# Performance work log

Hardware: AMD Instinct MI355X
Metric: run time of the kernel (lower is better)

The kernel has to match this reference:

```python
import jax, jax.numpy as jnp
import numpy as np

N_ITEMS = 100000
N_EDGES = 800000
D = 64
N_LAYERS = 3  # config['ii_layers']


def setup_inputs() -> dict:
    key = jax.random.key(0)
    k1, k2, k3, k4 = jax.random.split(key, 4)
    rows = jax.random.randint(k1, (N_EDGES,), 0, N_ITEMS, dtype=jnp.int64 if jax.config.jax_enable_x64 else jnp.int32)
    cols = jax.random.randint(k2, (N_EDGES,), 0, N_ITEMS, dtype=jnp.int64 if jax.config.jax_enable_x64 else jnp.int32)
    vals = jax.random.uniform(k3, (N_EDGES,), dtype=jnp.float32)
    item_embeddings = jax.random.normal(k4, (N_ITEMS, D), dtype=jnp.float32)
    return {"rows": rows, "cols": cols, "vals": vals, "item_embeddings": item_embeddings}


def _spmm(rows, cols, vals, x):
    # sparse.mm(A, x) with A in COO: out[r] += vals[e] * x[c] for each edge e=(r,c)
    msgs = vals[:, None] * x[cols]            # [E, D] gathered & weighted messages
    return jax.ops.segment_sum(msgs, rows, num_segments=N_ITEMS)


def reference(rows, cols, vals, item_embeddings):
    # HyperConv: iterate SpMM, average initial + all layer outputs (fused running sum).
    acc = item_embeddings
    cur = item_embeddings
    for _ in range(N_LAYERS):
        cur = _spmm(rows, cols, vals, cur)
        acc = acc + cur
    return acc / jnp.asarray(N_LAYERS + 1, dtype=item_embeddings.dtype)
```

## Files before the change

kernel.cpp:

```cpp
#include <hip/hip_runtime.h>
#include <hip/hip_fp16.h>


#define NI 100000
#define NE 800000
#define DD 64

#define RPB  512
#define BINS ((NI + RPB - 1) / RPB)
#define EPB  2048
#define P1B  ((NE + EPB - 1) / EPB)
#define CAP  5120
#define BC   32
#define CVB  6250
#define SPLIT 4
#define RQ   (RPB / SPLIT)

typedef int   i4 __attribute__((ext_vector_type(4)));
typedef float f4 __attribute__((ext_vector_type(4)));

static __device__ __forceinline__ float2 h2f(int w) {
    __half2 h = *(__half2*)&w;
    return __half22float2(h);
}

__global__ __launch_bounds__(256) void part1_conv_k(const int* __restrict__ rows,
                                                    const int* __restrict__ cols,
                                                    const float* __restrict__ vals,
                                                    int* __restrict__ bin_cnt,
                                                    int2* __restrict__ binned,
                                                    const float4* __restrict__ x,
                                                    __half* __restrict__ xh,
                                                    int n4) {
    int t = threadIdx.x;
    if (blockIdx.x >= P1B) {
        int i = (blockIdx.x - P1B) * 256 + t;
        if (i < n4) {
            float4 v = x[i];
            __half2* dst = (__half2*)(xh + (size_t)i * 4);
            dst[0] = __floats2half2_rn(v.x, v.y);
            dst[1] = __floats2half2_rn(v.z, v.w);
        }
        return;
    }

    __shared__ int  hist[BINS];
    __shared__ int  offs[BINS];
    __shared__ int  base[BINS];
    __shared__ int  cur[BINS];
    __shared__ int  sc[256];
    __shared__ int2 stage[EPB];
    __shared__ unsigned char sbin[EPB];

    int e0   = blockIdx.x * EPB;
    int ecnt = NE - e0; if (ecnt > EPB) ecnt = EPB;

    for (int i = t; i < BINS; i += 256) { hist[i] = 0; cur[i] = 0; }
    __syncthreads();
    for (int i = t; i < ecnt; i += 256)
        atomicAdd(&hist[rows[e0 + i] >> 9], 1);
    __syncthreads();

    int hv = (t < BINS) ? hist[t] : 0;
    sc[t] = hv;
    __syncthreads();
    for (int off = 1; off < 256; off <<= 1) {
        int xv = (t >= off) ? sc[t - off] : 0;
        __syncthreads();
        sc[t] += xv;
        __syncthreads();
    }
    if (t < BINS) {
        offs[t] = sc[t] - hv;
        base[t] = hv ? atomicAdd(&bin_cnt[t], hv) : 0;
    }
    __syncthreads();

    for (int i = t; i < ecnt; i += 256) {
        int r = rows[e0 + i];
        int b = r >> 9;
        int p = offs[b] + atomicAdd(&cur[b], 1);
        stage[p] = make_int2(((r & 511) << 17) | cols[e0 + i],
                             __float_as_int(vals[e0 + i]));
        sbin[p] = (unsigned char)b;
    }
    __syncthreads();

    for (int i = t; i < ecnt; i += 256) {
        int b   = sbin[i];
        int pos = base[b] + (i - offs[b]);
        if (pos < CAP) binned[(size_t)b * CAP + pos] = stage[i];
    }
}

__global__ __launch_bounds__(256) void part2_k(const int* __restrict__ bin_cnt,
                                               const int2* __restrict__ binned,
                                               int2* __restrict__ bucket,
                                               int* __restrict__ fill) {
    __shared__ int cur[RQ];
    int t  = threadIdx.x;
    int bb = blockIdx.x >> 2;
    int q  = blockIdx.x & 3;
    for (int i = t; i < RQ; i += 256) cur[i] = 0;
    __syncthreads();
    int cnt = bin_cnt[bb];
    if (cnt > CAP) cnt = CAP;
    const int2* src = binned + (size_t)bb * CAP;
    for (int i = t; i < cnt; i += 256) {
        int2 e = src[i];
        int rl = e.x >> 17;
        if ((rl >> 7) == q) {
            int pos = atomicAdd(&cur[rl & (RQ - 1)], 1);
            if (pos < BC)
                bucket[((size_t)bb * RPB + rl) * BC + pos] =
                    make_int2(e.x & 0x1FFFF, e.y);
        }
    }
    __syncthreads();
    for (int i = t; i < RQ; i += 256) {
        int rl = q * RQ + i;
        int r  = bb * RPB + rl;
        if (r < NI) {
            int c = (cur[i] < BC) ? cur[i] : BC;
            if (c & 1) {
                bucket[((size_t)bb * RPB + rl) * BC + c] = make_int2(0, 0);
                c++;
            }
            fill[r] = c;
        }
    }
}

template <int MODE>
__global__ __launch_bounds__(256, 8) void spmm_k(const int* __restrict__ fill,
                                                 const int2* __restrict__ bucket,
                                                 const __half* __restrict__ xin,
                                                 __half* __restrict__ nxt,
                                                 const float* __restrict__ x0,
                                                 const __half* __restrict__ s1,
                                                 float* __restrict__ outp) {
    int tid  = threadIdx.x;
    int lane = tid & 63;
    int grp  = lane >> 3;
    int ll   = lane & 7;
    int r    = blockIdx.x * 32 + (tid >> 6) * 8 + grp;
    int deg  = fill[r];
    const int2* ep = bucket + (size_t)r * BC;

    int wmax = deg;
    wmax = max(wmax, __shfl_xor(wmax, 8, 64));
    wmax = max(wmax, __shfl_xor(wmax, 16, 64));
    wmax = max(wmax, __shfl_xor(wmax, 32, 64));
    int wmax4 = (wmax + 3) & ~3;

    i4 q0 = (i4)0, q1 = (i4)0;
    if (2 * ll < deg)      q0 = __builtin_nontemporal_load((const i4*)(ep + 2 * ll));
    if (16 + 2 * ll < deg) q1 = __builtin_nontemporal_load((const i4*)(ep + 16 + 2 * ll));

    float a0 = 0.f, a1 = 0.f, a2 = 0.f, a3 = 0.f;
    float a4 = 0.f, a5 = 0.f, a6 = 0.f, a7 = 0.f;

    for (int j = 0; j < wmax4; j += 4) {
        int s0 = (lane & 56) | ((j >> 1) & 7);
        int s1i = s0 + 1;
        i4 qa = (j < 16) ? q0 : q1;
        int c0  = __shfl(qa[0], s0, 64);
        int v0i = __shfl(qa[1], s0, 64);
        int c1  = __shfl(qa[2], s0, 64);
        int v1i = __shfl(qa[3], s0, 64);
        int c2  = __shfl(qa[0], s1i, 64);
        int v2i = __shfl(qa[1], s1i, 64);
        int c3  = __shfl(qa[2], s1i, 64);
        int v3i = __shfl(qa[3], s1i, 64);

        i4 g0 = *(const i4*)(xin + (size_t)c0 * DD + 8 * ll);
        i4 g1 = *(const i4*)(xin + (size_t)c1 * DD + 8 * ll);
        i4 g2 = *(const i4*)(xin + (size_t)c2 * DD + 8 * ll);
        i4 g3 = *(const i4*)(xin + (size_t)c3 * DD + 8 * ll);

        float v0 = __int_as_float(v0i);
        float v1 = __int_as_float(v1i);
        float v2 = __int_as_float(v2i);
        float v3 = __int_as_float(v3i);
        float2 f;
        f = h2f(g0[0]); a0 += v0 * f.x; a1 += v0 * f.y;
        f = h2f(g0[1]); a2 += v0 * f.x; a3 += v0 * f.y;
        f = h2f(g0[2]); a4 += v0 * f.x; a5 += v0 * f.y;
        f = h2f(g0[3]); a6 += v0 * f.x; a7 += v0 * f.y;
        f = h2f(g1[0]); a0 += v1 * f.x; a1 += v1 * f.y;
        f = h2f(g1[1]); a2 += v1 * f.x; a3 += v1 * f.y;
        f = h2f(g1[2]); a4 += v1 * f.x; a5 += v1 * f.y;
        f = h2f(g1[3]); a6 += v1 * f.x; a7 += v1 * f.y;
        f = h2f(g2[0]); a0 += v2 * f.x; a1 += v2 * f.y;
        f = h2f(g2[1]); a2 += v2 * f.x; a3 += v2 * f.y;
        f = h2f(g2[2]); a4 += v2 * f.x; a5 += v2 * f.y;
        f = h2f(g2[3]); a6 += v2 * f.x; a7 += v2 * f.y;
        f = h2f(g3[0]); a0 += v3 * f.x; a1 += v3 * f.y;
        f = h2f(g3[1]); a2 += v3 * f.x; a3 += v3 * f.y;
        f = h2f(g3[2]); a4 += v3 * f.x; a5 += v3 * f.y;
        f = h2f(g3[3]); a6 += v3 * f.x; a7 += v3 * f.y;
    }

    if (MODE == 2) {
        size_t fo = (size_t)r * DD + 8 * ll;
        f4 xa = __builtin_nontemporal_load((const f4*)(x0 + fo));
        f4 xb = __builtin_nontemporal_load((const f4*)(x0 + fo) + 1);
        i4 s1u = __builtin_nontemporal_load((const i4*)(s1 + fo));
        i4 s2u = *(const i4*)(xin + fo);
        f4 oa, ob;
        float2 f1, f2;
        f1 = h2f(s1u[0]); f2 = h2f(s2u[0]);
        oa[0] = (xa[0] + f1.x + f2.x + a0) * 0.25f;
        oa[1] = (xa[1] + f1.y + f2.y + a1) * 0.25f;
        f1 = h2f(s1u[1]); f2 = h2f(s2u[1]);
        oa[2] = (xa[2] + f1.x + f2.x + a2) * 0.25f;
        oa[3] = (xa[3] + f1.y + f2.y + a3) * 0.25f;
        f1 = h2f(s1u[2]); f2 = h2f(s2u[2]);
        ob[0] = (xb[0] + f1.x + f2.x + a4) * 0.25f;
        ob[1] = (xb[1] + f1.y + f2.y + a5) * 0.25f;
        f1 = h2f(s1u[3]); f2 = h2f(s2u[3]);
        ob[2] = (xb[2] + f1.x + f2.x + a6) * 0.25f;
        ob[3] = (xb[3] + f1.y + f2.y + a7) * 0.25f;
        f4* op = (f4*)(outp + fo);
        __builtin_nontemporal_store(oa, op);
        __builtin_nontemporal_store(ob, op + 1);
    } else {
        i4 o;
        __half2 h;
        h = __floats2half2_rn(a0, a1); o[0] = *(int*)&h;
        h = __floats2half2_rn(a2, a3); o[1] = *(int*)&h;
        h = __floats2half2_rn(a4, a5); o[2] = *(int*)&h;
        h = __floats2half2_rn(a6, a7); o[3] = *(int*)&h;
        *(i4*)(nxt + (size_t)r * DD + 8 * ll) = o;
    }
}

#define NB ((NI + 255) / 256)

__global__ __launch_bounds__(256) void init_k(const float4* __restrict__ x,
                                              float4* __restrict__ cur,
                                              float4* __restrict__ acc, int n4) {
    int i = blockIdx.x * 256 + threadIdx.x;
    if (i < n4) { float4 v = x[i]; cur[i] = v; acc[i] = v; }
}

__global__ __launch_bounds__(256) void hist_k(const int* __restrict__ rows,
                                              int* __restrict__ counts) {
    int e = blockIdx.x * 256 + threadIdx.x;
    if (e < NE) atomicAdd(&counts[rows[e]], 1);
}

__global__ __launch_bounds__(256) void scan1_k(const int* __restrict__ counts,
                                               int* __restrict__ bsum) {
    __shared__ int s[256];
    int t = threadIdx.x;
    int i = blockIdx.x * 256 + t;
    s[t] = (i < NI) ? counts[i] : 0;
    __syncthreads();
    for (int off = 128; off > 0; off >>= 1) {
        if (t < off) s[t] += s[t + off];
        __syncthreads();
    }
    if (t == 0) bsum[blockIdx.x] = s[0];
}

__global__ __launch_bounds__(512) void scan2_k(int* __restrict__ bsum) {
    __shared__ int s[512];
    int t = threadIdx.x;
    int v = (t < NB) ? bsum[t] : 0;
    s[t] = v;
    __syncthreads();
    for (int off = 1; off < 512; off <<= 1) {
        int tmp = (t >= off) ? s[t - off] : 0;
        __syncthreads();
        s[t] += tmp;
        __syncthreads();
    }
    if (t < NB) bsum[t] = s[t] - v;
}

__global__ __launch_bounds__(256) void scan3_k(const int* __restrict__ counts,
                                               const int* __restrict__ bsum,
                                               int* __restrict__ rowptr) {
    __shared__ int s[256];
    int t = threadIdx.x;
    int i = blockIdx.x * 256 + t;
    int v = (i < NI) ? counts[i] : 0;
    s[t] = v;
    __syncthreads();
    for (int off = 1; off < 256; off <<= 1) {
        int tmp = (t >= off) ? s[t - off] : 0;
        __syncthreads();
        s[t] += tmp;
        __syncthreads();
    }
    int excl = s[t] - v + bsum[blockIdx.x];
    if (i < NI) rowptr[i] = excl;
    if (i == NI - 1) rowptr[NI] = excl + v;
}

__global__ __launch_bounds__(256) void scatter_k(const int* __restrict__ rows,
                                                 const int* __restrict__ cols,
                                                 const float* __restrict__ vals,
                                                 const int* __restrict__ rowptr,
                                                 int* __restrict__ fillc,
                                                 int2* __restrict__ edges) {
    int e = blockIdx.x * 256 + threadIdx.x;
    if (e < NE) {
        int r = rows[e];
        int pos = rowptr[r] + atomicAdd(&fillc[r], 1);
        edges[pos] = make_int2(cols[e], __float_as_int(vals[e]));
    }
}

__global__ __launch_bounds__(256) void spmm_csr_k(const int* __restrict__ rowptr,
                                                  const int2* __restrict__ edges,
                                                  const float* __restrict__ x,
                                                  float* __restrict__ nxt,
                                                  float* __restrict__ acc,
                                                  int last) {
    int r = __builtin_amdgcn_readfirstlane(blockIdx.x * 4 + (threadIdx.x >> 6));
    int lane = threadIdx.x & 63;
    int beg = rowptr[r];
    int end = rowptr[r + 1];
    float s = 0.f;
    int j = beg;
    for (; j + 3 < end; j += 4) {
        int2 e0 = edges[j], e1 = edges[j + 1], e2 = edges[j + 2], e3 = edges[j + 3];
        float g0 = x[(size_t)e0.x * DD + lane];
        float g1 = x[(size_t)e1.x * DD + lane];
        float g2 = x[(size_t)e2.x * DD + lane];
        float g3 = x[(size_t)e3.x * DD + lane];
        s += __int_as_float(e0.y) * g0; s += __int_as_float(e1.y) * g1;
        s += __int_as_float(e2.y) * g2; s += __int_as_float(e3.y) * g3;
    }
    for (; j < end; ++j) {
        int2 e = edges[j];
        s += __int_as_float(e.y) * x[(size_t)e.x * DD + lane];
    }
    size_t o = (size_t)r * DD + lane;
    if (last) acc[o] = (acc[o] + s) * 0.25f;
    else { nxt[o] = s; acc[o] += s; }
}

extern "C" void kernel_launch(void* const* d_in, const int* in_sizes, int n_in,
                              void* d_out, int out_size, void* d_ws, size_t ws_size,
                              hipStream_t stream) {
    const int*   rows = (const int*)d_in[0];
    const int*   cols = (const int*)d_in[1];
    const float* vals = (const float*)d_in[2];
    const float* x    = (const float*)d_in[3];
    float* outp = (float*)d_out;

    const size_t fbuf  = (size_t)NI * DD * sizeof(float);
    const size_t hbuf  = (size_t)NI * DD * sizeof(__half);
    const int    n4        = NI * DD / 4;
    const int    grid_elem = (n4 + 255) / 256;

    char* wsp = (char*)d_ws;

    size_t off_xh     = 0;
    size_t off_s1     = off_xh + hbuf;
    size_t off_s2     = off_s1 + hbuf;
    size_t off_bucket = off_s2 + hbuf;
    size_t off_binned = off_bucket + (size_t)NI * BC * 8;
    size_t off_fill   = off_binned + (size_t)BINS * CAP * 8;
    size_t off_bcnt   = off_fill + (size_t)NI * 4;
    size_t need       = off_bcnt + (size_t)BINS * 4;

    if (ws_size >= need) {
        __half* xh      = (__half*)(wsp + off_xh);
        __half* s1h     = (__half*)(wsp + off_s1);
        __half* s2h     = (__half*)(wsp + off_s2);
        int2*   bucket  = (int2*)(wsp + off_bucket);
        int2*   binned  = (int2*)(wsp + off_binned);
        int*    fill    = (int*)(wsp + off_fill);
        int*    bin_cnt = (int*)(wsp + off_bcnt);

        hipMemsetAsync(bin_cnt, 0, BINS * sizeof(int), stream);
        part1_conv_k<<<P1B + CVB, 256, 0, stream>>>(rows, cols, vals, bin_cnt, binned,
                                                    (const float4*)x, xh, n4);
        part2_k<<<BINS * SPLIT, 256, 0, stream>>>(bin_cnt, binned, bucket, fill);

        const int grid_spmm = NI / 32;
        spmm_k<0><<<grid_spmm, 256, 0, stream>>>(fill, bucket, xh,  s1h, nullptr, nullptr, nullptr);
        spmm_k<1><<<grid_spmm, 256, 0, stream>>>(fill, bucket, s1h, s2h, nullptr, nullptr, nullptr);
        spmm_k<2><<<grid_spmm, 256, 0, stream>>>(fill, bucket, s2h, nullptr, x, s1h, outp);
        return;
    }

    const int grid_edge = (NE + 255) / 256;
    const int grid_csr  = NI / 4;

    float* bufA   = (float*)wsp;
    float* bufB   = (float*)(wsp + fbuf);
    int2*  edges  = (int2*)(wsp + 2 * fbuf);
    int*   rowptr = (int*)(wsp + 2 * fbuf + (size_t)NE * 8);
    int*   counts = rowptr + (NI + 1);
    int*   bsum   = counts + NI;

    hipMemsetAsync(counts, 0, NI * sizeof(int), stream);
    hist_k<<<grid_edge, 256, 0, stream>>>(rows, counts);
    scan1_k<<<NB, 256, 0, stream>>>(counts, bsum);
    scan2_k<<<1, 512, 0, stream>>>(bsum);
    scan3_k<<<NB, 256, 0, stream>>>(counts, bsum, rowptr);
    hipMemsetAsync(counts, 0, NI * sizeof(int), stream);
    scatter_k<<<grid_edge, 256, 0, stream>>>(rows, cols, vals, rowptr, counts, edges);
    init_k<<<grid_elem, 256, 0, stream>>>((const float4*)x, (float4*)bufA,
                                          (float4*)outp, n4);
    spmm_csr_k<<<grid_csr, 256, 0, stream>>>(rowptr, edges, bufA, bufB, outp, 0);
    spmm_csr_k<<<grid_csr, 256, 0, stream>>>(rowptr, edges, bufB, bufA, outp, 0);
    spmm_csr_k<<<grid_csr, 256, 0, stream>>>(rowptr, edges, bufA, bufB, outp, 1);
}
```

Before: 170.9 us.

## Fuse bucket scatter with first SpMM layer in one kernel

Merges the per-row bucketing kernel with the first SpMM layer: each block, after building buckets for its 128 rows, immediately runs the SpMM for those four 32-row tiles. This removes one kernel launch and the inter-kernel gap, and reuses freshly written bucket data while it may still be in cache. In exchange the first layer runs with far fewer blocks, each doing serial work, which reduces parallelism and latency hiding.

```diff
diff --git a/kernel.cpp b/kernel.cpp
--- a/kernel.cpp
+++ b/kernel.cpp
@@ -6,15 +6,16 @@
 #define NE 800000
 #define DD 64
 
-#define RPB  512
-#define BINS ((NI + RPB - 1) / RPB)
-#define EPB  2048
-#define P1B  ((NE + EPB - 1) / EPB)
-#define CAP  5120
-#define BC   32
-#define CVB  6250
+#define RPB   512
+#define BINS  ((NI + RPB - 1) / RPB)
+#define EPB   2048
+#define P1B   ((NE + EPB - 1) / EPB)
+#define CAP   5120
+#define BC    32
+#define CVB   6250
 #define SPLIT 4
-#define RQ   (RPB / SPLIT)
+#define RQ    (RPB / SPLIT)
+#define NTILE (NI / 32)
 
 typedef int   i4 __attribute__((ext_vector_type(4)));
 typedef float f4 __attribute__((ext_vector_type(4)));
@@ -24,115 +25,8 @@
     return __half22float2(h);
 }
 
-__global__ __launch_bounds__(256) void part1_conv_k(const int* __restrict__ rows,
-                                                    const int* __restrict__ cols,
-                                                    const float* __restrict__ vals,
-                                                    int* __restrict__ bin_cnt,
-                                                    int2* __restrict__ binned,
-                                                    const float4* __restrict__ x,
-                                                    __half* __restrict__ xh,
-                                                    int n4) {
-    int t = threadIdx.x;
-    if (blockIdx.x >= P1B) {
-        int i = (blockIdx.x - P1B) * 256 + t;
-        if (i < n4) {
-            float4 v = x[i];
-            __half2* dst = (__half2*)(xh + (size_t)i * 4);
-            dst[0] = __floats2half2_rn(v.x, v.y);
-            dst[1] = __floats2half2_rn(v.z, v.w);
-        }
-        return;
-    }
-
-    __shared__ int  hist[BINS];
-    __shared__ int  offs[BINS];
-    __shared__ int  base[BINS];
-    __shared__ int  cur[BINS];
-    __shared__ int  sc[256];
-    __shared__ int2 stage[EPB];
-    __shared__ unsigned char sbin[EPB];
-
-    int e0   = blockIdx.x * EPB;
-    int ecnt = NE - e0; if (ecnt > EPB) ecnt = EPB;
-
-    for (int i = t; i < BINS; i += 256) { hist[i] = 0; cur[i] = 0; }
-    __syncthreads();
-    for (int i = t; i < ecnt; i += 256)
-        atomicAdd(&hist[rows[e0 + i] >> 9], 1);
-    __syncthreads();
-
-    int hv = (t < BINS) ? hist[t] : 0;
-    sc[t] = hv;
-    __syncthreads();
-    for (int off = 1; off < 256; off <<= 1) {
-        int xv = (t >= off) ? sc[t - off] : 0;
-        __syncthreads();
-        sc[t] += xv;
-        __syncthreads();
-    }
-    if (t < BINS) {
-        offs[t] = sc[t] - hv;
-        base[t] = hv ? atomicAdd(&bin_cnt[t], hv) : 0;
-    }
-    __syncthreads();
-
-    for (int i = t; i < ecnt; i += 256) {
-        int r = rows[e0 + i];
-        int b = r >> 9;
-        int p = offs[b] + atomicAdd(&cur[b], 1);
-        stage[p] = make_int2(((r & 511) << 17) | cols[e0 + i],
-                             __float_as_int(vals[e0 + i]));
-        sbin[p] = (unsigned char)b;
-    }
-    __syncthreads();
-
-    for (int i = t; i < ecnt; i += 256) {
-        int b   = sbin[i];
-        int pos = base[b] + (i - offs[b]);
-        if (pos < CAP) binned[(size_t)b * CAP + pos] = stage[i];
-    }
-}
-
-__global__ __launch_bounds__(256) void part2_k(const int* __restrict__ bin_cnt,
-                                               const int2* __restrict__ binned,
-                                               int2* __restrict__ bucket,
-                                               int* __restrict__ fill) {
-    __shared__ int cur[RQ];
-    int t  = threadIdx.x;
-    int bb = blockIdx.x >> 2;
-    int q  = blockIdx.x & 3;
-    for (int i = t; i < RQ; i += 256) cur[i] = 0;
-    __syncthreads();
-    int cnt = bin_cnt[bb];
-    if (cnt > CAP) cnt = CAP;
-    const int2* src = binned + (size_t)bb * CAP;
-    for (int i = t; i < cnt; i += 256) {
-        int2 e = src[i];
-        int rl = e.x >> 17;
-        if ((rl >> 7) == q) {
-            int pos = atomicAdd(&cur[rl & (RQ - 1)], 1);
-            if (pos < BC)
-                bucket[((size_t)bb * RPB + rl) * BC + pos] =
-                    make_int2(e.x & 0x1FFFF, e.y);
-        }
-    }
-    __syncthreads();
-    for (int i = t; i < RQ; i += 256) {
-        int rl = q * RQ + i;
-        int r  = bb * RPB + rl;
-        if (r < NI) {
-            int c = (cur[i] < BC) ? cur[i] : BC;
-            if (c & 1) {
-                bucket[((size_t)bb * RPB + rl) * BC + c] = make_int2(0, 0);
-                c++;
-            }
-            fill[r] = c;
-        }
-    }
-}
-
-template <int MODE>
-__global__ __launch_bounds__(256, 8) void spmm_k(const int* __restrict__ fill,
+static __device__ __forceinline__ void spmm_tile(int vb, int mode,
+                                                 const int* __restrict__ fill,
                                                  const int2* __restrict__ bucket,
                                                  const __half* __restrict__ xin,
                                                  __half* __restrict__ nxt,
@@ -143,7 +37,7 @@
     int lane = tid & 63;
     int grp  = lane >> 3;
     int ll   = lane & 7;
-    int r    = blockIdx.x * 32 + (tid >> 6) * 8 + grp;
+    int r    = vb * 32 + (tid >> 6) * 8 + grp;
     int deg  = fill[r];
     const int2* ep = bucket + (size_t)r * BC;
 
@@ -201,7 +95,7 @@
         f = h2f(g3[3]); a6 += v3 * f.x; a7 += v3 * f.y;
     }
 
-    if (MODE == 2) {
+    if (mode == 2) {
         size_t fo = (size_t)r * DD + 8 * ll;
         f4 xa = __builtin_nontemporal_load((const f4*)(x0 + fo));
         f4 xb = __builtin_nontemporal_load((const f4*)(x0 + fo) + 1);
@@ -235,6 +129,134 @@
     }
 }
 
+__global__ __launch_bounds__(256) void part1_conv_k(const int* __restrict__ rows,
+                                                    const int* __restrict__ cols,
+                                                    const float* __restrict__ vals,
+                                                    int* __restrict__ bin_cnt,
+                                                    int2* __restrict__ binned,
+                                                    const float4* __restrict__ x,
+                                                    __half* __restrict__ xh,
+                                                    int n4) {
+    int t = threadIdx.x;
+    if (blockIdx.x >= P1B) {
+        int i = (blockIdx.x - P1B) * 256 + t;
+        if (i < n4) {
+            float4 v = x[i];
+            __half2* dst = (__half2*)(xh + (size_t)i * 4);
+            dst[0] = __floats2half2_rn(v.x, v.y);
+            dst[1] = __floats2half2_rn(v.z, v.w);
+        }
+        return;
+    }
+
+    __shared__ int  hist[BINS];
+    __shared__ int  offs[BINS];
+    __shared__ int  base[BINS];
+    __shared__ int  cur[BINS];
+    __shared__ int  sc[256];
+    __shared__ int2 stage[EPB];
+    __shared__ unsigned char sbin[EPB];
+
+    int e0   = blockIdx.x * EPB;
+    int ecnt = NE - e0; if (ecnt > EPB) ecnt = EPB;
+
+    for (int i = t; i < BINS; i += 256) { hist[i] = 0; cur[i] = 0; }
+    __syncthreads();
+    for (int i = t; i < ecnt; i += 256)
+        atomicAdd(&hist[rows[e0 + i] >> 9], 1);
+    __syncthreads();
+
+    int hv = (t < BINS) ? hist[t] : 0;
+    sc[t] = hv;
+    __syncthreads();
+    for (int off = 1; off < 256; off <<= 1) {
+        int xv = (t >= off) ? sc[t - off] : 0;
+        __syncthreads();
+        sc[t] += xv;
+        __syncthreads();
+    }
+    if (t < BINS) {
+        offs[t] = sc[t] - hv;
+        base[t] = hv ? atomicAdd(&bin_cnt[t], hv) : 0;
+    }
+    __syncthreads();
+
+    for (int i = t; i < ecnt; i += 256) {
+        int r = rows[e0 + i];
+        int b = r >> 9;
+        int p = offs[b] + atomicAdd(&cur[b], 1);
+        stage[p] = make_int2(((r & 511) << 17) | cols[e0 + i],
+                             __float_as_int(vals[e0 + i]));
+        sbin[p] = (unsigned char)b;
+    }
+    __syncthreads();
+
+    for (int i = t; i < ecnt; i += 256) {
+        int b   = sbin[i];
+        int pos = base[b] + (i - offs[b]);
+        if (pos < CAP) binned[(size_t)b * CAP + pos] = stage[i];
+    }
+}
+
+__global__ __launch_bounds__(256, 8) void p2s0_k(const int* __restrict__ bin_cnt,
+                                                 const int2* __restrict__ binned,
+                                                 int2* __restrict__ bucket,
+                                                 int* __restrict__ fill,
+                                                 const __half* __restrict__ xh,
+                                                 __half* __restrict__ s1h) {
+    __shared__ int cur[RQ];
+    int t  = threadIdx.x;
+    int bb = blockIdx.x >> 2;
+    int q  = blockIdx.x & 3;
+    for (int i = t; i < RQ; i += 256) cur[i] = 0;
+    __syncthreads();
+    int cnt = bin_cnt[bb];
+    if (cnt > CAP) cnt = CAP;
+    const int2* src = binned + (size_t)bb * CAP;
+    for (int i = t; i < cnt; i += 256) {
+        int2 e = src[i];
+        int rl = e.x >> 17;
+        if ((rl >> 7) == q) {
+            int pos = atomicAdd(&cur[rl & (RQ - 1)], 1);
+            if (pos < BC)
+                bucket[((size_t)bb * RPB + rl) * BC + pos] =
+                    make_int2(e.x & 0x1FFFF, e.y);
+        }
+    }
+    __syncthreads();
+    for (int i = t; i < RQ; i += 256) {
+        int rl = q * RQ + i;
+        int r  = bb * RPB + rl;
+        if (r < NI) {
+            int c = (cur[i] < BC) ? cur[i] : BC;
+            if (c & 1) {
+                bucket[((size_t)bb * RPB + rl) * BC + c] = make_int2(0, 0);
+                c++;
+            }
+            fill[r] = c;
+        }
+    }
+    __syncthreads();
+
+    int vb0 = bb * 16 + q * 4;
+    for (int s = 0; s < 4; ++s) {
+        int vb = vb0 + s;
+        if (vb < NTILE)
+            spmm_tile(vb, 0, fill, bucket, xh, s1h, nullptr, nullptr, nullptr);
+    }
+}
+
+template <int MODE>
+__global__ __launch_bounds__(256, 8) void spmm_k(const int* __restrict__ fill,
+                                                 const int2* __restrict__ bucket,
+                                                 const __half* __restrict__ xin,
+                                                 __half* __restrict__ nxt,
+                                                 const float* __restrict__ x0,
+                                                 const __half* __restrict__ s1,
+                                                 float* __restrict__ outp) {
+    spmm_tile(blockIdx.x, MODE, fill, bucket, xin, nxt, x0, s1, outp);
+}
+
 #define NB ((NI + 255) / 256)
 
 __global__ __launch_bounds__(256) void init_k(const float4* __restrict__ x,
@@ -380,12 +402,10 @@
         hipMemsetAsync(bin_cnt, 0, BINS * sizeof(int), stream);
         part1_conv_k<<<P1B + CVB, 256, 0, stream>>>(rows, cols, vals, bin_cnt, binned,
                                                     (const float4*)x, xh, n4);
-        part2_k<<<BINS * SPLIT, 256, 0, stream>>>(bin_cnt, binned, bucket, fill);
-
-        const int grid_spmm = NI / 32;
-        spmm_k<0><<<grid_spmm, 256, 0, stream>>>(fill, bucket, xh,  s1h, nullptr, nullptr, nullptr);
-        spmm_k<1><<<grid_spmm, 256, 0, stream>>>(fill, bucket, s1h, s2h, nullptr, nullptr, nullptr);
-        spmm_k<2><<<grid_spmm, 256, 0, stream>>>(fill, bucket, s2h, nullptr, x, s1h, outp);
+        p2s0_k<<<BINS * SPLIT, 256, 0, stream>>>(bin_cnt, binned, bucket, fill,
+                                                 xh, s1h);
+        spmm_k<1><<<NTILE, 256, 0, stream>>>(fill, bucket, s1h, s2h, nullptr, nullptr, nullptr);
+        spmm_k<2><<<NTILE, 256, 0, stream>>>(fill, bucket, s2h, nullptr, x, s1h, outp);
         return;
     }
 
```

New measurement: 173.2 us. No clear change (+1.3%).
